# Kernel tuning notes

Measured on AMD Instinct MI355X. Metric: run time of the kernel, lower is better.

Reference implementation:

```python
import jax, jax.numpy as jnp
import numpy as np

NB, NLOC, NALL, NNEI = 1, 4096, 6144, 64
N_EDGE, N_ANGLE, A_SEL = 262144, 409600, 10
N_DIM, E_DIM, A_DIM, AXIS = 128, 64, 32, 4
SEL_REDUCE = 10.0


def _lin_params(key, din, dout):
    k1, k2 = jax.random.split(key)
    W = jax.random.normal(k1, (din, dout), jnp.float32) / np.float32(np.sqrt(din))
    b = jax.random.normal(k2, (dout,), jnp.float32) * 0.01
    return W, b


def setup_inputs():
    key = jax.random.key(0)
    ks = jax.random.split(key, 20)
    inp = {}
    inp["node_ebd_ext"] = jax.random.normal(ks[0], (NB, NALL, N_DIM), jnp.float32)
    inp["edge_ebd"] = jax.random.normal(ks[1], (N_EDGE, E_DIM), jnp.float32)
    inp["h2"] = jax.random.normal(ks[2], (N_EDGE, 3), jnp.float32)
    inp["angle_ebd"] = jax.random.normal(ks[3], (N_ANGLE, A_DIM), jnp.float32)
    inp["nlist"] = jax.random.randint(ks[4], (NB, NLOC, NNEI), 0, NALL)
    inp["nlist_mask"] = jnp.ones((NB, NLOC, NNEI), jnp.bool_)
    inp["sw"] = jax.random.uniform(ks[5], (N_EDGE,), jnp.float32)
    inp["a_nlist"] = jax.random.randint(ks[6], (NB, NLOC, A_SEL), 0, NALL)
    inp["a_nlist_mask"] = jnp.ones((NB, NLOC, A_SEL), jnp.bool_)
    inp["a_sw"] = jax.random.uniform(ks[7], (N_ANGLE,), jnp.float32)
    n2e = jax.random.randint(ks[8], (N_EDGE,), 0, NB * NLOC)
    n_ext2e = jax.random.randint(ks[9], (N_EDGE,), 0, NB * NALL)
    inp["edge_index"] = jnp.stack([n2e, n_ext2e])
    n2a = jax.random.randint(ks[10], (N_ANGLE,), 0, NB * NLOC)
    eij2a = jax.random.randint(ks[11], (N_ANGLE,), 0, N_EDGE)
    eik2a = jax.random.randint(ks[12], (N_ANGLE,), 0, N_EDGE)
    inp["angle_index"] = jnp.stack([n2a, eij2a, eik2a])
    sym_dim = (N_DIM + E_DIM) * AXIS          # 768
    edge_info_dim = 2 * N_DIM + E_DIM         # 320
    angle_dim = A_DIM + N_DIM + 2 * E_DIM     # 288
    inp["W_node_self"], inp["b_node_self"] = _lin_params(ks[13], N_DIM, N_DIM)
    inp["W_node_sym"], inp["b_node_sym"] = _lin_params(ks[14], sym_dim, N_DIM)
    inp["W_node_edge"], inp["b_node_edge"] = _lin_params(ks[15], edge_info_dim, N_DIM)
    inp["W_edge_self"], inp["b_edge_self"] = _lin_params(ks[16], edge_info_dim, E_DIM)
    inp["W_edge_angle1"], inp["b_edge_angle1"] = _lin_params(ks[17], angle_dim, E_DIM)
    inp["W_edge_angle2"], inp["b_edge_angle2"] = _lin_params(ks[18], E_DIM, E_DIM)
    inp["W_angle_self"], inp["b_angle_self"] = _lin_params(ks[19], angle_dim, A_DIM)
    inp["n_res0"] = jnp.full((N_DIM,), 0.1, jnp.float32)
    inp["n_res1"] = jnp.full((N_DIM,), 0.1, jnp.float32)
    inp["n_res2"] = jnp.full((N_DIM,), 0.1, jnp.float32)
    inp["e_res0"] = jnp.full((E_DIM,), 0.1, jnp.float32)
    inp["e_res1"] = jnp.full((E_DIM,), 0.1, jnp.float32)
    inp["a_res0"] = jnp.full((A_DIM,), 0.1, jnp.float32)
    return inp


def reference(node_ebd_ext, edge_ebd, h2, angle_ebd, nlist, nlist_mask, sw,
              a_nlist, a_nlist_mask, a_sw, edge_index, angle_index,
              W_node_self, b_node_self, W_node_sym, b_node_sym,
              W_node_edge, b_node_edge, W_edge_self, b_edge_self,
              W_edge_angle1, b_edge_angle1, W_edge_angle2, b_edge_angle2,
              W_angle_self, b_angle_self,
              n_res0, n_res1, n_res2, e_res0, e_res1, a_res0):
    act = jax.nn.silu
    nb, nloc, nnei = nlist.shape
    n_dim = node_ebd_ext.shape[-1]
    n_edge = h2.shape[0]
    dyn_e_sel = nnei / SEL_REDUCE
    dyn_a_sel = a_nlist.shape[-1] / SEL_REDUCE
    node_ebd = node_ebd_ext[:, :nloc]
    n2e, n_ext2e = edge_index[0], edge_index[1]
    n2a, eij2a, eik2a = angle_index[0], angle_index[1], angle_index[2]
    nei_node_ebd = node_ebd_ext.reshape(-1, n_dim)[n_ext2e]  # [n_edge, n_dim]
    node_self = act(node_ebd @ W_node_self + b_node_self)

    def sym_op(flat_ebd):
        # symmetrization: outer(h2, sw*ebd) scattered to owners, then grrg
        d = flat_ebd.shape[-1]
        w = flat_ebd * sw[:, None]
        h2g2 = jax.ops.segment_sum(
            (h2[:, :, None] * w[:, None, :]).reshape(n_edge, 3 * d),
            n2e, num_segments=nb * nloc)
        h2g2 = h2g2.reshape(nb, nloc, 3, d) * (dyn_e_sel ** -0.5)
        m = h2g2[..., :AXIS]  # [nb, nloc, 3, axis]
        g = jnp.einsum('blxa,blxd->blad', m, h2g2) / 3.0
        return g.reshape(nb, nloc, AXIS * d)

    sym_edge = sym_op(edge_ebd)
    sym_node = sym_op(nei_node_ebd)
    node_sym = act(jnp.concatenate([sym_edge, sym_node], -1) @ W_node_sym + b_node_sym)
    node_i = node_ebd.reshape(-1, n_dim)[n2e]
    edge_info = jnp.concatenate([node_i, nei_node_ebd, edge_ebd], -1)  # [n_edge, 320]
    node_edge_update = act(edge_info @ W_node_edge + b_node_edge) * sw[:, None]
    node_edge_msg = jax.ops.segment_sum(node_edge_update, n2e, num_segments=nb * nloc).reshape(nb, nloc, -1) / dyn_e_sel
    n_updated = node_ebd + n_res0 * node_self + n_res1 * node_sym + n_res2 * node_edge_msg
    edge_self = act(edge_info @ W_edge_self + b_edge_self)
    node_for_angle = node_ebd.reshape(-1, n_dim)[n2a]
    edge_ik = edge_ebd[eik2a]
    edge_ij = edge_ebd[eij2a]
    angle_info = jnp.concatenate([angle_ebd, node_for_angle, edge_ik, edge_ij], -1)  # [n_angle, 288]
    edge_angle = act(angle_info @ W_edge_angle1 + b_edge_angle1)
    reduced = jax.ops.segment_sum(edge_angle * a_sw[:, None], eij2a, num_segments=n_edge) / (dyn_a_sel ** 0.5)
    edge_angle_msg = act(reduced @ W_edge_angle2 + b_edge_angle2)
    e_updated = edge_ebd + e_res0 * edge_self + e_res1 * edge_angle_msg
    angle_self = act(angle_info @ W_angle_self + b_angle_self)
    a_updated = angle_ebd + a_res0 * angle_self
    return (n_updated, e_updated, a_updated)
```

## Files before the change

### kernel.cpp

```cpp
#include <hip/hip_runtime.h>
#include <hip/hip_bf16.h>

#define NLOC_   4096
#define NALL_   6144
#define NEDGE_  262144
#define NANGLE_ 409600

typedef __bf16 bf16x8 __attribute__((ext_vector_type(8)));
typedef float  f32x4  __attribute__((ext_vector_type(4)));
typedef unsigned short u16;

__device__ __forceinline__ float silu_(float x){ return x / (1.0f + __expf(-x)); }

__device__ __forceinline__ u16 f2bu(float f){
    union { float f; unsigned u; } v; v.f = f;
    unsigned r = v.u + 0x7fffu + ((v.u >> 16) & 1u);
    return (u16)(r >> 16);
}
__device__ __forceinline__ float bu2f(u16 b){
    union { unsigned u; float f; } v; v.u = ((unsigned)b) << 16; return v.f;
}
__device__ __forceinline__ void st_bf16x4(u16* dst, float4 v){
    unsigned lo = (unsigned)f2bu(v.x) | ((unsigned)f2bu(v.y) << 16);
    unsigned hi = (unsigned)f2bu(v.z) | ((unsigned)f2bu(v.w) << 16);
    *reinterpret_cast<uint2*>(dst) = make_uint2(lo, hi);
}

__global__ __launch_bounds__(256) void k_mega_prep(
    const float* __restrict__ Wne, const float* __restrict__ Wes,
    const float* __restrict__ W1,  const float* __restrict__ WA,
    const float* __restrict__ W2,  const float* __restrict__ Wsym,
    const float* __restrict__ Wns,
    const float* __restrict__ node_ext, const float* __restrict__ edge_ebd,
    const float* __restrict__ angle_ebd,
    const int* __restrict__ n2e, const int* __restrict__ eij2a,
    u16* __restrict__ WTe, u16* __restrict__ WTa2, u16* __restrict__ WTaN,
    u16* __restrict__ WT2, u16* __restrict__ WsymT, u16* __restrict__ WnsT,
    u16* __restrict__ NB, u16* __restrict__ EB, u16* __restrict__ AB,
    int* __restrict__ cnt, int* __restrict__ cnt2)
{
    const int b = blockIdx.x, tid = threadIdx.x;
    if (b < 812) {
        int i = b*256 + tid;
        if (i < 61440) {
            int r = i/320, c = i - r*320;
            WTe[i] = f2bu(r < 128 ? Wne[c*128 + r] : Wes[c*64 + (r-128)]);
        } else if (i < 76800) {
            int j = i - 61440; int r = j/160, c2 = j - r*160;
            int k = (c2 < 32) ? c2 : c2 + 128;
            WTa2[j] = f2bu(r < 64 ? W1[k*64 + r] : WA[k*32 + (r-64)]);
        } else if (i < 89088) {
            int j = i - 76800; int r = j >> 7, c2 = j & 127;
            int k = c2 + 32;
            WTaN[j] = f2bu(r < 64 ? W1[k*64 + r] : WA[k*32 + (r-64)]);
        } else if (i < 93184) {
            int j = i - 89088; int r = j >> 6, c = j & 63;
            WT2[j] = f2bu(W2[c*64 + r]);
        } else if (i < 191488) {
            int j = i - 93184; int r = j/768, c = j - r*768;
            WsymT[j] = f2bu(Wsym[c*128 + r]);
        } else {
            int j = i - 191488; int r = j >> 7, c = j & 127;
            WnsT[j] = f2bu(Wns[c*128 + r]);
        }
    } else if (b < 1580) {
        int i = (b - 812)*256 + tid;
        float4 v = ((const float4*)node_ext)[i];
        st_bf16x4(&NB[(size_t)i*4], v);
    } else if (b < 3628) {
        for (int i = (b - 1580)*256 + tid; i < NEDGE_*64/4; i += 2048*256) {
            float4 v = ((const float4*)edge_ebd)[i];
            st_bf16x4(&EB[(size_t)i*4], v);
        }
    } else if (b < 5676) {
        for (int i = (b - 3628)*256 + tid; i < NANGLE_*32/4; i += 2048*256) {
            float4 v = ((const float4*)angle_ebd)[i];
            st_bf16x4(&AB[(size_t)i*4], v);
        }
    } else if (b < 6700) {
        int e = (b - 5676)*256 + tid;
        atomicAdd(&cnt[n2e[e]], 1);
    } else {
        int a = (b - 6700)*256 + tid;
        atomicAdd(&cnt2[eij2a[a]], 1);
    }
}

__global__ __launch_bounds__(256) void k_scan_misc(
    const int* __restrict__ cnt, int* __restrict__ off, int* __restrict__ cursor,
    const int* __restrict__ cnt2, int* __restrict__ bsum,
    const u16* __restrict__ NB, const u16* __restrict__ WTe,
    const u16* __restrict__ WTaN,
    float* __restrict__ nconst, float* __restrict__ nconstA)
{
    __shared__ __align__(16) u16 sN[64][136];
    int* wa = (int*)&sN[0][0];
    const int b = blockIdx.x, t = threadIdx.x;

    if (b == 0) {
        int v[16]; int s = 0;
        #pragma unroll
        for (int k = 0; k < 16; ++k) { v[k] = s; s += cnt[16*t + k]; }
        wa[t] = s;
        __syncthreads();
        for (int d = 1; d < 256; d <<= 1) {
            int x = wa[t];
            int y = (t >= d) ? wa[t-d] : 0;
            __syncthreads();
            wa[t] = x + y;
            __syncthreads();
        }
        int excl = (t == 0) ? 0 : wa[t-1];
        #pragma unroll
        for (int k = 0; k < 16; ++k) {
            off[16*t + k]    = excl + v[k];
            cursor[16*t + k] = excl + v[k];
        }
        if (t == 255) off[4096] = excl + s;
    } else if (b <= 256) {
        int bb = b - 1;
        int4 v = ((const int4*)cnt2)[bb*256 + t];
        wa[t] = v.x + v.y + v.z + v.w;
        __syncthreads();
        for (int d = 128; d > 0; d >>= 1) {
            if (t < d) wa[t] += wa[t+d];
            __syncthreads();
        }
        if (t == 0) bsum[bb] = wa[0];
    } else if (b <= 320) {
        const int e0 = (b - 257) * 64;
        #pragma unroll
        for (int f = t; f < 1024; f += 256) {
            int r = f >> 4, c = f & 15;
            *(uint4*)&sN[r][8*c] = ((const uint4*)&NB[(size_t)(e0 + r)*128])[c];
        }
        __syncthreads();
// ... 52 lines not shown
            #pragma unroll
            for (int j = 0; j < 4; ++j) {
                int r = 16*w + 4*hq + j;
                nconstA[(size_t)(n0 + r)*96 + c] = acc[nf][j];
            }
        }
    }
}

__global__ void k_scan2b(const int* __restrict__ bsum, int* __restrict__ boff)
{
    __shared__ int wa[256];
    int t = threadIdx.x;
    wa[t] = bsum[t];
    __syncthreads();
    for (int d = 1; d < 256; d <<= 1) {
        int x = wa[t];
        int y = (t >= d) ? wa[t-d] : 0;
        __syncthreads();
        wa[t] = x + y;
        __syncthreads();
    }
    boff[t] = (t == 0) ? 0 : wa[t-1];
}

__global__ void k_scan2c(const int* __restrict__ cnt2, const int* __restrict__ boff,
                         int* __restrict__ off2, int* __restrict__ cursor2)
{
    __shared__ int wa[256];
    int b = blockIdx.x, t = threadIdx.x;
    int4 v = ((const int4*)cnt2)[b*256 + t];
    int s1 = v.x, s2 = s1 + v.y, s3 = s2 + v.z, s4 = s3 + v.w;
    wa[t] = s4;
    __syncthreads();
    for (int d = 1; d < 256; d <<= 1) {
        int x = wa[t];
        int y = (t >= d) ? wa[t-d] : 0;
        __syncthreads();
        wa[t] = x + y;
        __syncthreads();
    }
    int base = boff[b] + ((t == 0) ? 0 : wa[t-1]);
    int i = (b*256 + t)*4;
    off2[i]   = base;      cursor2[i]   = base;
    off2[i+1] = base + s1; cursor2[i+1] = base + s1;
    off2[i+2] = base + s2; cursor2[i+2] = base + s2;
    off2[i+3] = base + s3; cursor2[i+3] = base + s3;
    if (b == 255 && t == 255) off2[NEDGE_] = NANGLE_;
}

__global__ void k_fill2(const int* __restrict__ n2e, int* __restrict__ cursor,
                        int* __restrict__ csr,
                        const int* __restrict__ eij2a, int* __restrict__ cursor2,
                        int* __restrict__ csr2)
{
    int b = blockIdx.x;
    if (b < 1024) {
        int e = b*256 + threadIdx.x;
        int pos = atomicAdd(&cursor[n2e[e]], 1);
        csr[pos] = e;
    } else {
        int a = (b - 1024)*256 + threadIdx.x;
        int pos = atomicAdd(&cursor2[eij2a[a]], 1);
        csr2[pos] = a;
    }
}

__global__ __launch_bounds__(256, 4) void k_edge_flat(
    const u16* __restrict__ NB, const u16* __restrict__ EB,
    const float* __restrict__ h2, const float* __restrict__ sw,
    const int* __restrict__ n2e, const int* __restrict__ n_ext2e,
    const int* __restrict__ csr,
    const u16* __restrict__ WTe, const float* __restrict__ nconst,
    const float* __restrict__ bne, const float* __restrict__ bes,
    float* __restrict__ msg,
    float* __restrict__ h2g2_e, float* __restrict__ h2g2_n,
    u16* __restrict__ eselfO)
{
    __shared__ __align__(16) u16 sA[64][200];
    __shared__ float sH[4][576];
    __shared__ int   s_eid[64];
    __shared__ int   s_node[64];
    __shared__ int   s_g[64];
    __shared__ float s_sw[64];
    __shared__ float s_h2[64][3];
    __shared__ int   s_segstart[65];
    __shared__ int   s_nseg;

    const int tid = threadIdx.x;
    const int w  = tid >> 6, l = tid & 63;
    const int lr = l & 15, hq = l >> 4, lk = hq * 8;
    const int base = blockIdx.x * 64;

    if (tid < 64) {
        int e = csr[base + tid];
        s_eid[tid]  = e;
        s_node[tid] = n2e[e];
        s_g[tid]    = n_ext2e[e];
        s_sw[tid]   = sw[e];
        s_h2[tid][0] = h2[e*3];
        s_h2[tid][1] = h2[e*3+1];
        s_h2[tid][2] = h2[e*3+2];
    }
    __syncthreads();

    if (tid < 64) {
        bool flag = (tid == 0) || (s_node[tid] != s_node[tid-1]);
        unsigned long long mask = __ballot(flag);
        if (flag) {
            int sid = __popcll(mask & ((1ull << tid) - 1ull));
            s_segstart[sid] = tid;
        }
        if (tid == 0) {
            int ns = __popcll(mask);
            s_nseg = ns;
            s_segstart[ns] = 64;
        }
    }

    #pragma unroll
    for (int f = tid; f < 1024; f += 256) {
        int r = f >> 4, c = f & 15;
        *(uint4*)&sA[r][8*c] = ((const uint4*)&NB[(size_t)s_g[r]*128])[c];
    }
    #pragma unroll
    for (int f = tid; f < 512; f += 256) {
        int r = f >> 3, c = f & 7;
        *(uint4*)&sA[r][128 + 8*c] = ((const uint4*)&EB[(size_t)s_eid[r]*64])[c];
    }
    __syncthreads();

    float bias[3];
    int   cful[3];
    #pragma unroll
    for (int nf = 0; nf < 3; ++nf) {
        int c = 48*w + 16*nf + lr;
        cful[nf] = c;
        bias[nf] = (c < 128) ? bne[c] : bes[c-128];
    }

    f32x4 acc[4][3] = {};
    #pragma unroll
    for (int kk = 0; kk < 6; ++kk) {
        bf16x8 a[4], b[3];
        #pragma unroll
        for (int m = 0; m < 4; ++m)
            a[m] = *(const bf16x8*)&sA[16*m + lr][kk*32 + lk];
        #pragma unroll
        for (int nf = 0; nf < 3; ++nf)
            b[nf] = *(const bf16x8*)&WTe[(size_t)cful[nf]*320 + 128 + kk*32 + lk];
        #pragma unroll
        for (int m = 0; m < 4; ++m)
            #pragma unroll
            for (int nf = 0; nf < 3; ++nf)
                acc[m][nf] = __builtin_amdgcn_mfma_f32_16x16x32_bf16(a[m], b[nf], acc[m][nf], 0, 0, 0);
    }

    #pragma unroll
    for (int nf = 0; nf < 3; ++nf) {
        int c = cful[nf];
        if (c < 128) {
            #pragma unroll
            for (int m = 0; m < 4; ++m)
                #pragma unroll
                for (int j = 0; j < 4; ++j) {
                    int r = 16*m + 4*hq + j;
                    float ncv = nconst[(size_t)s_node[r]*192 + c];
                    acc[m][nf][j] = silu_(acc[m][nf][j] + ncv + bias[nf]) * s_sw[r];
                }
        } else {
            int c2 = c - 128;
            #pragma unroll
            for (int m = 0; m < 4; ++m)
                #pragma unroll
                for (int j = 0; j < 4; ++j) {
                    int r = 16*m + 4*hq + j;
                    float ncv = nconst[(size_t)s_node[r]*192 + c];
                    eselfO[(size_t)s_eid[r]*64 + c2] =
                        f2bu(silu_(acc[m][nf][j] + ncv + bias[nf]));
                }
        }
    }

    const int nseg = s_nseg;
    for (int s = 0; s < nseg; ++s) {
        int rs = s_segstart[s], re = s_segstart[s+1];
        int nd = s_node[rs];
        #pragma unroll
        for (int nf = 0; nf < 3; ++nf) {
            if (cful[nf] >= 128) continue;
            float v = 0.f;
            #pragma unroll
            for (int m = 0; m < 4; ++m)
                #pragma unroll
                for (int j = 0; j < 4; ++j) {
                    int r = 16*m + 4*hq + j;
                    v += (r >= rs && r < re) ? acc[m][nf][j] : 0.f;
                }
            v += __shfl_xor(v, 16);
            v += __shfl_xor(v, 32);
            if (hq == 0) atomicAdd(&msg[(size_t)nd*128 + cful[nf]], v);
        }
    }

    for (int s = 0; s < nseg; ++s) {
        int rs = s_segstart[s], re = s_segstart[s+1];
        int nd = s_node[rs];
        int lo = max(16*w, rs), hi = min(16*w + 16, re);
        float hacc[9] = {0.f,0.f,0.f,0.f,0.f,0.f,0.f,0.f,0.f};
        for (int r = lo; r < hi; ++r) {
            float swv = s_sw[r];
            float s0 = s_h2[r][0] * swv;
            float s1 = s_h2[r][1] * swv;
            float s2 = s_h2[r][2] * swv;
            float eb = bu2f(sA[r][128 + l]);
            float n0 = bu2f(sA[r][l]);
            float n1 = bu2f(sA[r][64 + l]);
            hacc[0] = fmaf(s0, eb, hacc[0]);
            hacc[1] = fmaf(s1, eb, hacc[1]);
            hacc[2] = fmaf(s2, eb, hacc[2]);
            hacc[3] = fmaf(s0, n0, hacc[3]);
            hacc[4] = fmaf(s0, n1, hacc[4]);
            hacc[5] = fmaf(s1, n0, hacc[5]);
            hacc[6] = fmaf(s1, n1, hacc[6]);
            hacc[7] = fmaf(s2, n0, hacc[7]);
            hacc[8] = fmaf(s2, n1, hacc[8]);
        }
        #pragma unroll
        for (int q = 0; q < 3; ++q) sH[w][q*64 + l] = hacc[q];
        #pragma unroll
        for (int q = 0; q < 6; ++q) sH[w][192 + q*64 + l] = hacc[3+q];
        __syncthreads();
        for (int i = tid; i < 576; i += 256) {
            float v = sH[0][i] + sH[1][i] + sH[2][i] + sH[3][i];
            if (i < 192) atomicAdd(&h2g2_e[(size_t)nd*192 + i], v);
            else         atomicAdd(&h2g2_n[(size_t)nd*384 + (i - 192)], v);
        }
        __syncthreads();
    }
}

__global__ __launch_bounds__(256) void k_angle_mfma(
    const u16* __restrict__ EB, const u16* __restrict__ AB,
    const float* __restrict__ a_sw,
    const int* __restrict__ n2a, const int* __restrict__ eij2a,
    const int* __restrict__ eik2a, const int* __restrict__ csr2,
    const u16* __restrict__ WTa2, const float* __restrict__ nconstA,
    const float* __restrict__ b1, const float* __restrict__ bA,
    const float* __restrict__ a_res0,
    u16* __restrict__ ea, float* __restrict__ a_out)
{
    __shared__ __align__(16) u16 sA[32][168];
    __shared__ __align__(16) u16 sEA[32][64];
    __shared__ int s_a[32], s_nd[32], s_ij[32], s_ik[32];
    __shared__ float s_asw[32];
    const int tid = threadIdx.x;
    const int p0 = blockIdx.x * 32;

    if (tid < 32) {
        int a = csr2[p0 + tid];
        s_a[tid]  = a;
        s_nd[tid] = n2a[a];
        s_ij[tid] = eij2a[a];
        s_ik[tid] = eik2a[a];
        s_asw[tid] = a_sw[a];
    }
    __syncthreads();

    if (tid < 128) {
        int r = tid >> 2, c = tid & 3;
        *(uint4*)&sA[r][8*c] = ((const uint4*)&AB[(size_t)s_a[r]*32])[c];
    }
    {
        int r = tid >> 3, c = tid & 7;
        *(uint4*)&sA[r][32 + 8*c] = ((const uint4*)&EB[(size_t)s_ik[r]*64])[c];
        *(uint4*)&sA[r][96 + 8*c] = ((const uint4*)&EB[(size_t)s_ij[r]*64])[c];
    }
    __syncthreads();

    const int w = tid >> 6, l = tid & 63;
    const int lr = l & 15, hq = l >> 4, lk = hq * 8;
    const int mrow  = (w & 1) * 16;
    const int nbase = (w >> 1) * 48;

    f32x4 acc[3] = {};
    #pragma unroll
    for (int kk = 0; kk < 5; ++kk) {
        bf16x8 a = *(const bf16x8*)&sA[mrow + lr][kk*32 + lk];
        #pragma unroll
        for (int nf = 0; nf < 3; ++nf) {
            bf16x8 b = *(const bf16x8*)&WTa2[(size_t)(nbase + 16*nf + lr)*160 + kk*32 + lk];
            acc[nf] = __builtin_amdgcn_mfma_f32_16x16x32_bf16(a, b, acc[nf], 0, 0, 0);
        }
    }

    #pragma unroll
    for (int nf = 0; nf < 3; ++nf) {
        int c = nbase + 16*nf + lr;
        if (c < 64) {
            float bb = b1[c];
            #pragma unroll
            for (int j = 0; j < 4; ++j) {
                int r = mrow + 4*hq + j;
                float nca = nconstA[(size_t)s_nd[r]*96 + c];
                sEA[r][c] = f2bu(silu_(acc[nf][j] + nca + bb) * s_asw[r]);
            }
        } else {
            int c2 = c - 64;
            float bb = bA[c2], rr = a_res0[c2];
            #pragma unroll
            for (int j = 0; j < 4; ++j) {
                int r = mrow + 4*hq + j;
                float nca = nconstA[(size_t)s_nd[r]*96 + c];
                a_out[(size_t)s_a[r]*32 + c2] =
                    bu2f(sA[r][c2]) + rr * silu_(acc[nf][j] + nca + bb);
            }
        }
    }
    __syncthreads();

    {
        int r = tid >> 3, c = tid & 7;
        *(uint4*)&ea[((size_t)(p0 + r))*64 + 8*c] = *(const uint4*)&sEA[r][8*c];
    }
}

__global__ __launch_bounds__(256) void k_fin(
    const u16* __restrict__ EB, const u16* __restrict__ eselfO,
    const u16* __restrict__ ea, const int* __restrict__ off2,
    const u16* __restrict__ WT2,
    const float* __restrict__ b2_, const float* __restrict__ er0,
    const float* __restrict__ er1,
    float* __restrict__ e_out,
    const float* __restrict__ h2g2_e, const float* __restrict__ h2g2_n,
    u16* __restrict__ symcB)
{
    __shared__ __align__(16) u16 sR[64][72];
    __shared__ __align__(16) u16 sE[64][72];
    __shared__ __align__(16) u16 sB[64][72];
    const int tid = threadIdx.x;
    const int blk = blockIdx.x;

    if (blk < 4096) {
        const int e0 = blk * 64;
        const int w = tid >> 6, l = tid & 63;

        #pragma unroll
        for (int f = tid; f < 512; f += 256) {
            int r = f >> 3, c = f & 7;
            *(uint4*)&sB[r][8*c] = ((const uint4*)&EB[(size_t)(e0 + r)*64])[c];
            *(uint4*)&sE[r][8*c] = ((const uint4*)&eselfO[(size_t)(e0 + r)*64])[c];
        }

        #pragma unroll
        for (int r16 = 0; r16 < 16; ++r16) {
            int r = w*16 + r16;
            int e = e0 + r;
            float s = 0.f;
            int jb = off2[e], je = off2[e+1];
            for (int j = jb; j < je; ++j)
                s += bu2f(ea[(size_t)j*64 + l]);
            sR[r][l] = f2bu(s);
        }
        __syncthreads();

        const int lr = l & 15, hq = l >> 4, lk = hq * 8;
        f32x4 acc[4] = {};
        #pragma unroll
        for (int kk = 0; kk < 2; ++kk) {
            bf16x8 b = *(const bf16x8*)&WT2[(size_t)(16*w + lr)*64 + kk*32 + lk];
            #pragma unroll
            for (int m = 0; m < 4; ++m) {
                bf16x8 a = *(const bf16x8*)&sR[16*m + lr][kk*32 + lk];
                acc[m] = __builtin_amdgcn_mfma_f32_16x16x32_bf16(a, b, acc[m], 0, 0, 0);
            }
        }
// ... 110 lines not shown
            for (int j = 0; j < 4; ++j) {
                int r = 16*m + 4*hq + j;
                size_t idx = (size_t)(n0 + r)*128 + c;
                float self_ = silu_(accS[m][nf][j] + bS);
                float sym_  = silu_(accY[m][nf][j] + bY);
                n_out[idx] = node_ext[idx] + r0*self_ + r1*sym_
                           + r2 * msg[idx] * (1.0f / 6.4f);
            }
    }
}

extern "C" void kernel_launch(void* const* d_in, const int* in_sizes, int n_in,
                              void* d_out, int out_size, void* d_ws, size_t ws_size,
                              hipStream_t stream)
{
    const float* node_ext  = (const float*)d_in[0];
    const float* edge_ebd  = (const float*)d_in[1];
    const float* h2        = (const float*)d_in[2];
    const float* angle_ebd = (const float*)d_in[3];
    const float* sw        = (const float*)d_in[6];
    const float* a_sw      = (const float*)d_in[9];
    const int*  edge_index  = (const int*)d_in[10];
    const int*  angle_index = (const int*)d_in[11];
    const int* n2e     = edge_index;
    const int* n_ext2e = edge_index + NEDGE_;
    const int* n2a     = angle_index;
    const int* eij2a   = angle_index + NANGLE_;
    const int* eik2a   = angle_index + 2*NANGLE_;

    const float* Wns  = (const float*)d_in[12];
    const float* bns  = (const float*)d_in[13];
    const float* Wsym = (const float*)d_in[14];
    const float* bsym = (const float*)d_in[15];
    const float* Wne  = (const float*)d_in[16];
    const float* bne  = (const float*)d_in[17];
    const float* Wes  = (const float*)d_in[18];
    const float* bes  = (const float*)d_in[19];
    const float* W1   = (const float*)d_in[20];
    const float* b1   = (const float*)d_in[21];
    const float* W2   = (const float*)d_in[22];
    const float* b2_  = (const float*)d_in[23];
    const float* WA   = (const float*)d_in[24];
    const float* bA   = (const float*)d_in[25];
    const float* nr0  = (const float*)d_in[26];
    const float* nr1  = (const float*)d_in[27];
    const float* nr2  = (const float*)d_in[28];
    const float* er0  = (const float*)d_in[29];
    const float* er1  = (const float*)d_in[30];
    const float* ar0  = (const float*)d_in[31];

    char* wsp = (char*)d_ws;
    u16*   ea      = (u16*)wsp;    wsp += (size_t)NANGLE_ * 64 * 2;
    u16*   EB      = (u16*)wsp;    wsp += (size_t)NEDGE_ * 64 * 2;
    u16*   NB      = (u16*)wsp;    wsp += (size_t)NALL_ * 128 * 2;
    u16*   AB      = (u16*)wsp;    wsp += (size_t)NANGLE_ * 32 * 2;
    u16*   eselfO  = (u16*)wsp;    wsp += (size_t)NEDGE_ * 64 * 2;
    u16*   symcB   = (u16*)wsp;    wsp += (size_t)NLOC_ * 768 * 2;
    int*   cnt     = (int*)wsp;    wsp += 4096 * 4;
    int*   cnt2    = (int*)wsp;    wsp += (size_t)NEDGE_ * 4;
    float* msg     = (float*)wsp;  wsp += (size_t)NLOC_ * 128 * 4;
    float* h2g2_e  = (float*)wsp;  wsp += (size_t)NLOC_ * 192 * 4;
    float* h2g2_n  = (float*)wsp;  wsp += (size_t)NLOC_ * 384 * 4;
    size_t zero_bytes = 4096*4 + (size_t)NEDGE_*4 + (size_t)NLOC_*128*4
                      + (size_t)NLOC_*192*4 + (size_t)NLOC_*384*4;
    int*   off     = (int*)wsp;    wsp += 4104 * 4;
    int*   cursor  = (int*)wsp;    wsp += 4096 * 4;
    int*   csr     = (int*)wsp;    wsp += (size_t)NEDGE_ * 4;
    int*   off2    = (int*)wsp;    wsp += ((size_t)NEDGE_ + 16) * 4;
    int*   cursor2 = (int*)wsp;    wsp += (size_t)NEDGE_ * 4;
    int*   bsum    = (int*)wsp;    wsp += 256 * 4;
    int*   boff    = (int*)wsp;    wsp += 256 * 4;
    int*   csr2    = (int*)wsp;    wsp += (size_t)NANGLE_ * 4;
    float* nconst  = (float*)wsp;  wsp += (size_t)NLOC_ * 192 * 4;
    float* nconstA = (float*)wsp;  wsp += (size_t)NLOC_ * 96 * 4;
    u16*   WTe     = (u16*)wsp;    wsp += 192 * 320 * 2;
    u16*   WTa2    = (u16*)wsp;    wsp += 96 * 160 * 2;
    u16*   WTaN    = (u16*)wsp;    wsp += 96 * 128 * 2;
    u16*   WT2     = (u16*)wsp;    wsp += 64 * 64 * 2;
    u16*   WsymT   = (u16*)wsp;    wsp += 128 * 768 * 2;
    u16*   WnsT    = (u16*)wsp;    wsp += 128 * 128 * 2;

    hipMemsetAsync(cnt, 0, zero_bytes, stream);

    float* n_out = (float*)d_out;
    float* e_out = n_out + (size_t)NLOC_ * 128;
    float* a_out = e_out + (size_t)NEDGE_ * 64;

    k_mega_prep <<<8300, 256, 0, stream>>>(Wne, Wes, W1, WA, W2, Wsym, Wns,
                                           node_ext, edge_ebd, angle_ebd,
                                           n2e, eij2a,
                                           WTe, WTa2, WTaN, WT2, WsymT, WnsT,
                                           NB, EB, AB, cnt, cnt2);
    k_scan_misc <<<385, 256, 0, stream>>>(cnt, off, cursor, cnt2, bsum,
                                          NB, WTe, WTaN, nconst, nconstA);
    k_scan2b <<<1, 256, 0, stream>>>(bsum, boff);
    k_scan2c <<<256, 256, 0, stream>>>(cnt2, boff, off2, cursor2);
    k_fill2  <<<2624, 256, 0, stream>>>(n2e, cursor, csr, eij2a, cursor2, csr2);

    k_edge_flat <<<NEDGE_/64, 256, 0, stream>>>(NB, EB, h2, sw, n2e, n_ext2e, csr,
                                                WTe, nconst, bne, bes,
                                                msg, h2g2_e, h2g2_n, eselfO);
    k_angle_mfma <<<NANGLE_/32, 256, 0, stream>>>(EB, AB, a_sw,
                                                  n2a, eij2a, eik2a, csr2,
                                                  WTa2, nconstA, b1, bA, ar0,
                                                  ea, a_out);
    k_fin <<<8192, 256, 0, stream>>>(EB, eselfO, ea, off2, WT2, b2_, er0, er1,
                                     e_out, h2g2_e, h2g2_n, symcB);
    k_node_mfma <<<NLOC_/32, 256, 0, stream>>>(symcB, NB, node_ext, msg,
                                               WsymT, WnsT, bns, bsym,
                                               nr0, nr1, nr2, n_out);
}
```

Baseline: 422.6 us.

## Drop angle bf16 prepass, scatter edge rows in CSR order, stage nconst in LDS

Removes the separate bf16 conversion pass for angle embeddings; the angle kernel now converts gathered fp32 rows inline. The CSR fill kernel also copies each edge's bf16 row into a CSR-ordered buffer, so the edge kernel reads contiguous rows instead of gathering. The edge kernel computes segment IDs with a shuffle (removing one barrier) and caches per-segment nconst rows in reused LDS for up to 12 segments, falling back to global loads beyond that. The trade-offs are an extra 32MB scatter-copy, an extra barrier before sH is reused, and wider fp32 gathers in the angle kernel.

```diff
diff --git a/kernel.cpp b/kernel.cpp
--- a/kernel.cpp
+++ b/kernel.cpp
@@ -32,11 +32,10 @@
     const float* __restrict__ W2,  const float* __restrict__ Wsym,
     const float* __restrict__ Wns,
     const float* __restrict__ node_ext, const float* __restrict__ edge_ebd,
-    const float* __restrict__ angle_ebd,
     const int* __restrict__ n2e, const int* __restrict__ eij2a,
     u16* __restrict__ WTe, u16* __restrict__ WTa2, u16* __restrict__ WTaN,
     u16* __restrict__ WT2, u16* __restrict__ WsymT, u16* __restrict__ WnsT,
-    u16* __restrict__ NB, u16* __restrict__ EB, u16* __restrict__ AB,
+    u16* __restrict__ NB, u16* __restrict__ EB,
     int* __restrict__ cnt, int* __restrict__ cnt2)
 {
     const int b = blockIdx.x, tid = threadIdx.x;
@@ -72,16 +71,11 @@
             float4 v = ((const float4*)edge_ebd)[i];
             st_bf16x4(&EB[(size_t)i*4], v);
         }
-    } else if (b < 5676) {
-        for (int i = (b - 3628)*256 + tid; i < NANGLE_*32/4; i += 2048*256) {
-            float4 v = ((const float4*)angle_ebd)[i];
-            st_bf16x4(&AB[(size_t)i*4], v);
-        }
-    } else if (b < 6700) {
-        int e = (b - 5676)*256 + tid;
+    } else if (b < 4652) {
+        int e = (b - 3628)*256 + tid;
         atomicAdd(&cnt[n2e[e]], 1);
     } else {
-        int a = (b - 6700)*256 + tid;
+        int a = (b - 4652)*256 + tid;
         atomicAdd(&cnt2[eij2a[a]], 1);
     }
 }
@@ -240,13 +234,18 @@
 __global__ void k_fill2(const int* __restrict__ n2e, int* __restrict__ cursor,
                         int* __restrict__ csr,
                         const int* __restrict__ eij2a, int* __restrict__ cursor2,
-                        int* __restrict__ csr2)
+                        int* __restrict__ csr2,
+                        const u16* __restrict__ EB, u16* __restrict__ EBs)
 {
     int b = blockIdx.x;
     if (b < 1024) {
         int e = b*256 + threadIdx.x;
         int pos = atomicAdd(&cursor[n2e[e]], 1);
         csr[pos] = e;
+        const uint4* src = (const uint4*)&EB[(size_t)e*64];
+        uint4* dst = (uint4*)&EBs[(size_t)pos*64];
+        #pragma unroll
+        for (int c = 0; c < 8; ++c) dst[c] = src[c];
     } else {
         int a = (b - 1024)*256 + threadIdx.x;
         int pos = atomicAdd(&cursor2[eij2a[a]], 1);
@@ -255,7 +254,7 @@
 }
 
 __global__ __launch_bounds__(256, 4) void k_edge_flat(
-    const u16* __restrict__ NB, const u16* __restrict__ EB,
+    const u16* __restrict__ NB, const u16* __restrict__ EBs,
     const float* __restrict__ h2, const float* __restrict__ sw,
     const int* __restrict__ n2e, const int* __restrict__ n_ext2e,
     const int* __restrict__ csr,
@@ -266,13 +265,14 @@
     u16* __restrict__ eselfO)
 {
     __shared__ __align__(16) u16 sA[64][200];
-    __shared__ float sH[4][576];
+    __shared__ __align__(16) float sH[4][576];
     __shared__ int   s_eid[64];
     __shared__ int   s_node[64];
     __shared__ int   s_g[64];
     __shared__ float s_sw[64];
     __shared__ float s_h2[64][3];
     __shared__ int   s_segstart[65];
+    __shared__ int   s_segid[64];
     __shared__ int   s_nseg;
 
     const int tid = threadIdx.x;
@@ -282,29 +282,29 @@
 
     if (tid < 64) {
         int e = csr[base + tid];
+        int nd = n2e[e];
         s_eid[tid]  = e;
-        s_node[tid] = n2e[e];
+        s_node[tid] = nd;
         s_g[tid]    = n_ext2e[e];
         s_sw[tid]   = sw[e];
         s_h2[tid][0] = h2[e*3];
         s_h2[tid][1] = h2[e*3+1];
         s_h2[tid][2] = h2[e*3+2];
-    }
-    __syncthreads();
-
-    if (tid < 64) {
-        bool flag = (tid == 0) || (s_node[tid] != s_node[tid-1]);
+        int ndp = __shfl_up(nd, 1);
+        bool flag = (tid == 0) || (nd != ndp);
         unsigned long long mask = __ballot(flag);
         if (flag) {
             int sid = __popcll(mask & ((1ull << tid) - 1ull));
             s_segstart[sid] = tid;
         }
+        s_segid[tid] = __popcll(mask & ((1ull << tid) | ((1ull << tid) - 1ull))) - 1;
         if (tid == 0) {
             int ns = __popcll(mask);
             s_nseg = ns;
             s_segstart[ns] = 64;
         }
     }
+    __syncthreads();
 
     #pragma unroll
     for (int f = tid; f < 1024; f += 256) {
@@ -314,7 +314,15 @@
     #pragma unroll
     for (int f = tid; f < 512; f += 256) {
         int r = f >> 3, c = f & 7;
-        *(uint4*)&sA[r][128 + 8*c] = ((const uint4*)&EB[(size_t)s_eid[r]*64])[c];
+        *(uint4*)&sA[r][128 + 8*c] = ((const uint4*)&EBs[(size_t)(base + r)*64])[c];
+    }
+    {
+        float* sNC = (float*)&sH[0][0];
+        int nsg = min(s_nseg, 12);
+        for (int i = tid; i < nsg*192; i += 256) {
+            int sgi = i / 192, c = i - sgi*192;
+            sNC[i] = nconst[(size_t)s_node[s_segstart[sgi]]*192 + c];
+        }
     }
     __syncthreads();
 
@@ -344,6 +352,7 @@
                 acc[m][nf] = __builtin_amdgcn_mfma_f32_16x16x32_bf16(a[m], b[nf], acc[m][nf], 0, 0, 0);
     }
 
+    const float* sNC = (const float*)&sH[0][0];
     #pragma unroll
     for (int nf = 0; nf < 3; ++nf) {
         int c = cful[nf];
@@ -353,7 +362,10 @@
                 #pragma unroll
                 for (int j = 0; j < 4; ++j) {
                     int r = 16*m + 4*hq + j;
-                    float ncv = nconst[(size_t)s_node[r]*192 + c];
+                    int sgi = s_segid[r];
+                    float ncv;
+                    if (sgi < 12) ncv = sNC[sgi*192 + c];
+                    else          ncv = nconst[(size_t)s_node[r]*192 + c];
                     acc[m][nf][j] = silu_(acc[m][nf][j] + ncv + bias[nf]) * s_sw[r];
                 }
         } else {
@@ -363,7 +375,10 @@
                 #pragma unroll
                 for (int j = 0; j < 4; ++j) {
                     int r = 16*m + 4*hq + j;
-                    float ncv = nconst[(size_t)s_node[r]*192 + c];
+                    int sgi = s_segid[r];
+                    float ncv;
+                    if (sgi < 12) ncv = sNC[sgi*192 + c];
+                    else          ncv = nconst[(size_t)s_node[r]*192 + c];
                     eselfO[(size_t)s_eid[r]*64 + c2] =
                         f2bu(silu_(acc[m][nf][j] + ncv + bias[nf]));
                 }
@@ -390,6 +405,8 @@
             if (hq == 0) atomicAdd(&msg[(size_t)nd*128 + cful[nf]], v);
         }
     }
+
+    __syncthreads();
 
     for (int s = 0; s < nseg; ++s) {
         int rs = s_segstart[s], re = s_segstart[s+1];
@@ -429,7 +446,7 @@
 }
 
 __global__ __launch_bounds__(256) void k_angle_mfma(
-    const u16* __restrict__ EB, const u16* __restrict__ AB,
+    const u16* __restrict__ EB, const float* __restrict__ angle_ebd,
     const float* __restrict__ a_sw,
     const int* __restrict__ n2a, const int* __restrict__ eij2a,
     const int* __restrict__ eik2a, const int* __restrict__ csr2,
@@ -455,9 +472,9 @@
     }
     __syncthreads();
 
-    if (tid < 128) {
-        int r = tid >> 2, c = tid & 3;
-        *(uint4*)&sA[r][8*c] = ((const uint4*)&AB[(size_t)s_a[r]*32])[c];
+    {
+        int r = tid >> 3, c = tid & 7;
+        st_bf16x4(&sA[r][4*c], ((const float4*)angle_ebd)[(size_t)s_a[r]*8 + c]);
     }
     {
         int r = tid >> 3, c = tid & 7;
@@ -726,8 +743,8 @@
     char* wsp = (char*)d_ws;
     u16*   ea      = (u16*)wsp;    wsp += (size_t)NANGLE_ * 64 * 2;
     u16*   EB      = (u16*)wsp;    wsp += (size_t)NEDGE_ * 64 * 2;
+    u16*   EBs     = (u16*)wsp;    wsp += (size_t)NEDGE_ * 64 * 2;
     u16*   NB      = (u16*)wsp;    wsp += (size_t)NALL_ * 128 * 2;
-    u16*   AB      = (u16*)wsp;    wsp += (size_t)NANGLE_ * 32 * 2;
     u16*   eselfO  = (u16*)wsp;    wsp += (size_t)NEDGE_ * 64 * 2;
     u16*   symcB   = (u16*)wsp;    wsp += (size_t)NLOC_ * 768 * 2;
     int*   cnt     = (int*)wsp;    wsp += 4096 * 4;
@@ -760,21 +777,22 @@
     float* e_out = n_out + (size_t)NLOC_ * 128;
     float* a_out = e_out + (size_t)NEDGE_ * 64;
 
-    k_mega_prep <<<8300, 256, 0, stream>>>(Wne, Wes, W1, WA, W2, Wsym, Wns,
-                                           node_ext, edge_ebd, angle_ebd,
+    k_mega_prep <<<6252, 256, 0, stream>>>(Wne, Wes, W1, WA, W2, Wsym, Wns,
+                                           node_ext, edge_ebd,
                                            n2e, eij2a,
                                            WTe, WTa2, WTaN, WT2, WsymT, WnsT,
-                                           NB, EB, AB, cnt, cnt2);
+                                           NB, EB, cnt, cnt2);
     k_scan_misc <<<385, 256, 0, stream>>>(cnt, off, cursor, cnt2, bsum,
                                           NB, WTe, WTaN, nconst, nconstA);
     k_scan2b <<<1, 256, 0, stream>>>(bsum, boff);
     k_scan2c <<<256, 256, 0, stream>>>(cnt2, boff, off2, cursor2);
-    k_fill2  <<<2624, 256, 0, stream>>>(n2e, cursor, csr, eij2a, cursor2, csr2);
-
-    k_edge_flat <<<NEDGE_/64, 256, 0, stream>>>(NB, EB, h2, sw, n2e, n_ext2e, csr,
+    k_fill2  <<<2624, 256, 0, stream>>>(n2e, cursor, csr, eij2a, cursor2, csr2,
+                                        EB, EBs);
+
+    k_edge_flat <<<NEDGE_/64, 256, 0, stream>>>(NB, EBs, h2, sw, n2e, n_ext2e, csr,
                                                 WTe, nconst, bne, bes,
                                                 msg, h2g2_e, h2g2_n, eselfO);
-    k_angle_mfma <<<NANGLE_/32, 256, 0, stream>>>(EB, AB, a_sw,
+    k_angle_mfma <<<NANGLE_/32, 256, 0, stream>>>(EB, angle_ebd, a_sw,
                                                   n2a, eij2a, eik2a, csr2,
                                                   WTa2, nconstA, b1, bA, ar0,
                                                   ea, a_out);
```

After: 459.9 us. +8.8%, slower.

## Merge edge and angle kernels into one interleaved launch, drop angle bf16 precast

Applied to the files above, without the earlier changes.

Fuses the edge-message kernel and the angle MFMA kernel into a single launch whose blocks are interleaved (one edge block per three angle blocks, then trailing angle blocks). Angle embeddings are now read as fp32 directly and converted to bf16 while being staged into shared memory, so the separate bf16 copy of angle_ebd in the prep kernel and its workspace buffer are removed. This saves one kernel launch and a full read and write of the angle tensor, and lets the two workloads overlap on the GPU. In exchange, the angle blocks now carry the edge kernel's larger shared-memory footprint and register budget, which may lower their occupancy.

```diff
diff --git a/kernel.cpp b/kernel.cpp
--- a/kernel.cpp
+++ b/kernel.cpp
@@ -32,11 +32,10 @@
     const float* __restrict__ W2,  const float* __restrict__ Wsym,
     const float* __restrict__ Wns,
     const float* __restrict__ node_ext, const float* __restrict__ edge_ebd,
-    const float* __restrict__ angle_ebd,
     const int* __restrict__ n2e, const int* __restrict__ eij2a,
     u16* __restrict__ WTe, u16* __restrict__ WTa2, u16* __restrict__ WTaN,
     u16* __restrict__ WT2, u16* __restrict__ WsymT, u16* __restrict__ WnsT,
-    u16* __restrict__ NB, u16* __restrict__ EB, u16* __restrict__ AB,
+    u16* __restrict__ NB, u16* __restrict__ EB,
     int* __restrict__ cnt, int* __restrict__ cnt2)
 {
     const int b = blockIdx.x, tid = threadIdx.x;
@@ -72,16 +71,11 @@
             float4 v = ((const float4*)edge_ebd)[i];
             st_bf16x4(&EB[(size_t)i*4], v);
         }
-    } else if (b < 5676) {
-        for (int i = (b - 3628)*256 + tid; i < NANGLE_*32/4; i += 2048*256) {
-            float4 v = ((const float4*)angle_ebd)[i];
-            st_bf16x4(&AB[(size_t)i*4], v);
-        }
-    } else if (b < 6700) {
-        int e = (b - 5676)*256 + tid;
+    } else if (b < 4652) {
+        int e = (b - 3628)*256 + tid;
         atomicAdd(&cnt[n2e[e]], 1);
     } else {
-        int a = (b - 6700)*256 + tid;
+        int a = (b - 4652)*256 + tid;
         atomicAdd(&cnt2[eij2a[a]], 1);
     }
 }
@@ -254,7 +248,7 @@
     }
 }
 
-__global__ __launch_bounds__(256, 4) void k_edge_flat(
+__global__ __launch_bounds__(256, 4) void k_edge_angle(
     const u16* __restrict__ NB, const u16* __restrict__ EB,
     const float* __restrict__ h2, const float* __restrict__ sw,
     const int* __restrict__ n2e, const int* __restrict__ n_ext2e,
@@ -263,10 +257,17 @@
     const float* __restrict__ bne, const float* __restrict__ bes,
     float* __restrict__ msg,
     float* __restrict__ h2g2_e, float* __restrict__ h2g2_n,
-    u16* __restrict__ eselfO)
+    u16* __restrict__ eselfO,
+    const float* __restrict__ angle_ebd, const float* __restrict__ a_sw,
+    const int* __restrict__ n2a, const int* __restrict__ eij2a,
+    const int* __restrict__ eik2a, const int* __restrict__ csr2,
+    const u16* __restrict__ WTa2, const float* __restrict__ nconstA,
+    const float* __restrict__ b1, const float* __restrict__ bA,
+    const float* __restrict__ a_res0,
+    u16* __restrict__ ea, float* __restrict__ a_out)
 {
     __shared__ __align__(16) u16 sA[64][200];
-    __shared__ float sH[4][576];
+    __shared__ __align__(16) float sH[4][576];
     __shared__ int   s_eid[64];
     __shared__ int   s_node[64];
     __shared__ int   s_g[64];
@@ -274,242 +275,238 @@
     __shared__ float s_h2[64][3];
     __shared__ int   s_segstart[65];
     __shared__ int   s_nseg;
+    __shared__ int   s_a[32], s_nd[32], s_ij[32], s_ik[32];
+    __shared__ float s_asw[32];
 
     const int tid = threadIdx.x;
+    const int b = blockIdx.x;
+    bool isEdge; int widx;
+    if (b < 16384) {
+        if ((b & 3) == 0) { isEdge = true;  widx = b >> 2; }
+        else              { isEdge = false; widx = b - (b >> 2) - 1; }
+    } else { isEdge = false; widx = 12288 + (b - 16384); }
+
     const int w  = tid >> 6, l = tid & 63;
     const int lr = l & 15, hq = l >> 4, lk = hq * 8;
-    const int base = blockIdx.x * 64;
-
-    if (tid < 64) {
-        int e = csr[base + tid];
-        s_eid[tid]  = e;
-        s_node[tid] = n2e[e];
-        s_g[tid]    = n_ext2e[e];
-        s_sw[tid]   = sw[e];
-        s_h2[tid][0] = h2[e*3];
-        s_h2[tid][1] = h2[e*3+1];
-        s_h2[tid][2] = h2[e*3+2];
-    }
-    __syncthreads();
-
-    if (tid < 64) {
-        bool flag = (tid == 0) || (s_node[tid] != s_node[tid-1]);
-        unsigned long long mask = __ballot(flag);
-        if (flag) {
-            int sid = __popcll(mask & ((1ull << tid) - 1ull));
-            s_segstart[sid] = tid;
-        }
-        if (tid == 0) {
-            int ns = __popcll(mask);
-            s_nseg = ns;
-            s_segstart[ns] = 64;
-        }
-    }
-
-    #pragma unroll
-    for (int f = tid; f < 1024; f += 256) {
-        int r = f >> 4, c = f & 15;
-        *(uint4*)&sA[r][8*c] = ((const uint4*)&NB[(size_t)s_g[r]*128])[c];
-    }
-    #pragma unroll
-    for (int f = tid; f < 512; f += 256) {
-        int r = f >> 3, c = f & 7;
-        *(uint4*)&sA[r][128 + 8*c] = ((const uint4*)&EB[(size_t)s_eid[r]*64])[c];
-    }
-    __syncthreads();
-
-    float bias[3];
-    int   cful[3];
-    #pragma unroll
-    for (int nf = 0; nf < 3; ++nf) {
-        int c = 48*w + 16*nf + lr;
-        cful[nf] = c;
-        bias[nf] = (c < 128) ? bne[c] : bes[c-128];
-    }
-
-    f32x4 acc[4][3] = {};
-    #pragma unroll
-    for (int kk = 0; kk < 6; ++kk) {
-        bf16x8 a[4], b[3];
-        #pragma unroll
-        for (int m = 0; m < 4; ++m)
-            a[m] = *(const bf16x8*)&sA[16*m + lr][kk*32 + lk];
-        #pragma unroll
-        for (int nf = 0; nf < 3; ++nf)
-            b[nf] = *(const bf16x8*)&WTe[(size_t)cful[nf]*320 + 128 + kk*32 + lk];
-        #pragma unroll
-        for (int m = 0; m < 4; ++m)
+
+    if (isEdge) {
+        const int base = widx * 64;
+
+        if (tid < 64) {
+            int e = csr[base + tid];
+            s_eid[tid]  = e;
+            s_node[tid] = n2e[e];
+            s_g[tid]    = n_ext2e[e];
+            s_sw[tid]   = sw[e];
+            s_h2[tid][0] = h2[e*3];
+            s_h2[tid][1] = h2[e*3+1];
+            s_h2[tid][2] = h2[e*3+2];
+        }
+        __syncthreads();
+
+        if (tid < 64) {
+            bool flag = (tid == 0) || (s_node[tid] != s_node[tid-1]);
+            unsigned long long mask = __ballot(flag);
+            if (flag) {
+                int sid = __popcll(mask & ((1ull << tid) - 1ull));
+                s_segstart[sid] = tid;
+            }
+            if (tid == 0) {
+                int ns = __popcll(mask);
+                s_nseg = ns;
+                s_segstart[ns] = 64;
+            }
+        }
+
+        #pragma unroll
+        for (int f = tid; f < 1024; f += 256) {
+            int r = f >> 4, c = f & 15;
+            *(uint4*)&sA[r][8*c] = ((const uint4*)&NB[(size_t)s_g[r]*128])[c];
+        }
+        #pragma unroll
+        for (int f = tid; f < 512; f += 256) {
+            int r = f >> 3, c = f & 7;
+            *(uint4*)&sA[r][128 + 8*c] = ((const uint4*)&EB[(size_t)s_eid[r]*64])[c];
+        }
+        __syncthreads();
+
+        float bias[3];
+        int   cful[3];
+        #pragma unroll
+        for (int nf = 0; nf < 3; ++nf) {
+            int c = 48*w + 16*nf + lr;
+            cful[nf] = c;
+            bias[nf] = (c < 128) ? bne[c] : bes[c-128];
+        }
+
+        f32x4 acc[4][3] = {};
+        #pragma unroll
+        for (int kk = 0; kk < 6; ++kk) {
+            bf16x8 a[4], bb[3];
+            #pragma unroll
+            for (int m = 0; m < 4; ++m)
+                a[m] = *(const bf16x8*)&sA[16*m + lr][kk*32 + lk];
             #pragma unroll
             for (int nf = 0; nf < 3; ++nf)
-                acc[m][nf] = __builtin_amdgcn_mfma_f32_16x16x32_bf16(a[m], b[nf], acc[m][nf], 0, 0, 0);
-    }
-
-    #pragma unroll
-    for (int nf = 0; nf < 3; ++nf) {
-        int c = cful[nf];
-        if (c < 128) {
+                bb[nf] = *(const bf16x8*)&WTe[(size_t)cful[nf]*320 + 128 + kk*32 + lk];
             #pragma unroll
             for (int m = 0; m < 4; ++m)
                 #pragma unroll
+                for (int nf = 0; nf < 3; ++nf)
+                    acc[m][nf] = __builtin_amdgcn_mfma_f32_16x16x32_bf16(a[m], bb[nf], acc[m][nf], 0, 0, 0);
+        }
+
+        #pragma unroll
+        for (int nf = 0; nf < 3; ++nf) {
+            int c = cful[nf];
+            if (c < 128) {
+                #pragma unroll
+                for (int m = 0; m < 4; ++m)
+                    #pragma unroll
+                    for (int j = 0; j < 4; ++j) {
+                        int r = 16*m + 4*hq + j;
+                        float ncv = nconst[(size_t)s_node[r]*192 + c];
+                        acc[m][nf][j] = silu_(acc[m][nf][j] + ncv + bias[nf]) * s_sw[r];
+                    }
+            } else {
+                int c2 = c - 128;
+                #pragma unroll
+                for (int m = 0; m < 4; ++m)
+                    #pragma unroll
+                    for (int j = 0; j < 4; ++j) {
+                        int r = 16*m + 4*hq + j;
+                        float ncv = nconst[(size_t)s_node[r]*192 + c];
+                        eselfO[(size_t)s_eid[r]*64 + c2] =
+                            f2bu(silu_(acc[m][nf][j] + ncv + bias[nf]));
+                    }
+            }
+        }
+
+        const int nseg = s_nseg;
+        for (int s = 0; s < nseg; ++s) {
+            int rs = s_segstart[s], re = s_segstart[s+1];
+            int nd = s_node[rs];
+            #pragma unroll
+            for (int nf = 0; nf < 3; ++nf) {
+                if (cful[nf] >= 128) continue;
+                float v = 0.f;
+                #pragma unroll
+                for (int m = 0; m < 4; ++m)
+                    #pragma unroll
+                    for (int j = 0; j < 4; ++j) {
+                        int r = 16*m + 4*hq + j;
+                        v += (r >= rs && r < re) ? acc[m][nf][j] : 0.f;
+                    }
+                v += __shfl_xor(v, 16);
+                v += __shfl_xor(v, 32);
+                if (hq == 0) atomicAdd(&msg[(size_t)nd*128 + cful[nf]], v);
+            }
+        }
+
+        for (int s = 0; s < nseg; ++s) {
+            int rs = s_segstart[s], re = s_segstart[s+1];
+            int nd = s_node[rs];
+            int lo = max(16*w, rs), hi = min(16*w + 16, re);
+            float hacc[9] = {0.f,0.f,0.f,0.f,0.f,0.f,0.f,0.f,0.f};
+            for (int r = lo; r < hi; ++r) {
+                float swv = s_sw[r];
+                float s0 = s_h2[r][0] * swv;
+                float s1 = s_h2[r][1] * swv;
+                float s2 = s_h2[r][2] * swv;
+                float eb = bu2f(sA[r][128 + l]);
+                float n0 = bu2f(sA[r][l]);
+                float n1 = bu2f(sA[r][64 + l]);
+                hacc[0] = fmaf(s0, eb, hacc[0]);
+                hacc[1] = fmaf(s1, eb, hacc[1]);
+                hacc[2] = fmaf(s2, eb, hacc[2]);
+                hacc[3] = fmaf(s0, n0, hacc[3]);
+                hacc[4] = fmaf(s0, n1, hacc[4]);
+                hacc[5] = fmaf(s1, n0, hacc[5]);
+                hacc[6] = fmaf(s1, n1, hacc[6]);
+                hacc[7] = fmaf(s2, n0, hacc[7]);
+                hacc[8] = fmaf(s2, n1, hacc[8]);
+            }
+            #pragma unroll
+            for (int q = 0; q < 3; ++q) sH[w][q*64 + l] = hacc[q];
+            #pragma unroll
+            for (int q = 0; q < 6; ++q) sH[w][192 + q*64 + l] = hacc[3+q];
+            __syncthreads();
+            for (int i = tid; i < 576; i += 256) {
+                float v = sH[0][i] + sH[1][i] + sH[2][i] + sH[3][i];
+                if (i < 192) atomicAdd(&h2g2_e[(size_t)nd*192 + i], v);
+                else         atomicAdd(&h2g2_n[(size_t)nd*384 + (i - 192)], v);
+            }
+            __syncthreads();
+        }
+    } else {
+        u16 (*sA32)[168] = (u16(*)[168])&sA[0][0];
+        u16 (*sEA)[64]   = (u16(*)[64])&sH[0][0];
+        const int p0 = widx * 32;
+
+        if (tid < 32) {
+            int a = csr2[p0 + tid];
+            s_a[tid]  = a;
+            s_nd[tid] = n2a[a];
+            s_ij[tid] = eij2a[a];
+            s_ik[tid] = eik2a[a];
+            s_asw[tid] = a_sw[a];
+        }
+        __syncthreads();
+
+        {
+            int r = tid >> 3, c = tid & 7;
+            st_bf16x4(&sA32[r][4*c], ((const float4*)angle_ebd)[(size_t)s_a[r]*8 + c]);
+        }
+        {
+            int r = tid >> 3, c = tid & 7;
+            *(uint4*)&sA32[r][32 + 8*c] = ((const uint4*)&EB[(size_t)s_ik[r]*64])[c];
+            *(uint4*)&sA32[r][96 + 8*c] = ((const uint4*)&EB[(size_t)s_ij[r]*64])[c];
+        }
+        __syncthreads();
+
+        const int mrow  = (w & 1) * 16;
+        const int nbase = (w >> 1) * 48;
+
+        f32x4 acc[3] = {};
+        #pragma unroll
+        for (int kk = 0; kk < 5; ++kk) {
+            bf16x8 a = *(const bf16x8*)&sA32[mrow + lr][kk*32 + lk];
+            #pragma unroll
+            for (int nf = 0; nf < 3; ++nf) {
+                bf16x8 bb = *(const bf16x8*)&WTa2[(size_t)(nbase + 16*nf + lr)*160 + kk*32 + lk];
+                acc[nf] = __builtin_amdgcn_mfma_f32_16x16x32_bf16(a, bb, acc[nf], 0, 0, 0);
+            }
+        }
+
+        #pragma unroll
+        for (int nf = 0; nf < 3; ++nf) {
+            int c = nbase + 16*nf + lr;
+            if (c < 64) {
+                float bb = b1[c];
+                #pragma unroll
                 for (int j = 0; j < 4; ++j) {
-                    int r = 16*m + 4*hq + j;
-                    float ncv = nconst[(size_t)s_node[r]*192 + c];
-                    acc[m][nf][j] = silu_(acc[m][nf][j] + ncv + bias[nf]) * s_sw[r];
+                    int r = mrow + 4*hq + j;
+                    float nca = nconstA[(size_t)s_nd[r]*96 + c];
+                    sEA[r][c] = f2bu(silu_(acc[nf][j] + nca + bb) * s_asw[r]);
                 }
-        } else {
-            int c2 = c - 128;
-            #pragma unroll
-            for (int m = 0; m < 4; ++m)
+            } else {
+                int c2 = c - 64;
+                float bb = bA[c2], rr = a_res0[c2];
                 #pragma unroll
                 for (int j = 0; j < 4; ++j) {
-                    int r = 16*m + 4*hq + j;
-                    float ncv = nconst[(size_t)s_node[r]*192 + c];
-                    eselfO[(size_t)s_eid[r]*64 + c2] =
-                        f2bu(silu_(acc[m][nf][j] + ncv + bias[nf]));
+                    int r = mrow + 4*hq + j;
+                    float nca = nconstA[(size_t)s_nd[r]*96 + c];
+                    a_out[(size_t)s_a[r]*32 + c2] =
+                        bu2f(sA32[r][c2]) + rr * silu_(acc[nf][j] + nca + bb);
                 }
-        }
-    }
-
-    const int nseg = s_nseg;
-    for (int s = 0; s < nseg; ++s) {
-        int rs = s_segstart[s], re = s_segstart[s+1];
-        int nd = s_node[rs];
-        #pragma unroll
-        for (int nf = 0; nf < 3; ++nf) {
-            if (cful[nf] >= 128) continue;
-            float v = 0.f;
-            #pragma unroll
-            for (int m = 0; m < 4; ++m)
-                #pragma unroll
-                for (int j = 0; j < 4; ++j) {
-                    int r = 16*m + 4*hq + j;
-                    v += (r >= rs && r < re) ? acc[m][nf][j] : 0.f;
-                }
-            v += __shfl_xor(v, 16);
-            v += __shfl_xor(v, 32);
-            if (hq == 0) atomicAdd(&msg[(size_t)nd*128 + cful[nf]], v);
-        }
-    }
-
-    for (int s = 0; s < nseg; ++s) {
-        int rs = s_segstart[s], re = s_segstart[s+1];
-        int nd = s_node[rs];
-        int lo = max(16*w, rs), hi = min(16*w + 16, re);
-        float hacc[9] = {0.f,0.f,0.f,0.f,0.f,0.f,0.f,0.f,0.f};
-        for (int r = lo; r < hi; ++r) {
-            float swv = s_sw[r];
-            float s0 = s_h2[r][0] * swv;
-            float s1 = s_h2[r][1] * swv;
-            float s2 = s_h2[r][2] * swv;
-            float eb = bu2f(sA[r][128 + l]);
-            float n0 = bu2f(sA[r][l]);
-            float n1 = bu2f(sA[r][64 + l]);
-            hacc[0] = fmaf(s0, eb, hacc[0]);
-            hacc[1] = fmaf(s1, eb, hacc[1]);
-            hacc[2] = fmaf(s2, eb, hacc[2]);
-            hacc[3] = fmaf(s0, n0, hacc[3]);
-            hacc[4] = fmaf(s0, n1, hacc[4]);
-            hacc[5] = fmaf(s1, n0, hacc[5]);
-            hacc[6] = fmaf(s1, n1, hacc[6]);
-            hacc[7] = fmaf(s2, n0, hacc[7]);
-            hacc[8] = fmaf(s2, n1, hacc[8]);
-        }
-        #pragma unroll
-        for (int q = 0; q < 3; ++q) sH[w][q*64 + l] = hacc[q];
-        #pragma unroll
-        for (int q = 0; q < 6; ++q) sH[w][192 + q*64 + l] = hacc[3+q];
-        __syncthreads();
-        for (int i = tid; i < 576; i += 256) {
-            float v = sH[0][i] + sH[1][i] + sH[2][i] + sH[3][i];
-            if (i < 192) atomicAdd(&h2g2_e[(size_t)nd*192 + i], v);
-            else         atomicAdd(&h2g2_n[(size_t)nd*384 + (i - 192)], v);
-        }
-        __syncthreads();
-    }
-}
-
-__global__ __launch_bounds__(256) void k_angle_mfma(
-    const u16* __restrict__ EB, const u16* __restrict__ AB,
-    const float* __restrict__ a_sw,
-    const int* __restrict__ n2a, const int* __restrict__ eij2a,
-    const int* __restrict__ eik2a, const int* __restrict__ csr2,
-    const u16* __restrict__ WTa2, const float* __restrict__ nconstA,
-    const float* __restrict__ b1, const float* __restrict__ bA,
-    const float* __restrict__ a_res0,
-    u16* __restrict__ ea, float* __restrict__ a_out)
-{
-    __shared__ __align__(16) u16 sA[32][168];
-    __shared__ __align__(16) u16 sEA[32][64];
-    __shared__ int s_a[32], s_nd[32], s_ij[32], s_ik[32];
-    __shared__ float s_asw[32];
-    const int tid = threadIdx.x;
-    const int p0 = blockIdx.x * 32;
-
-    if (tid < 32) {
-        int a = csr2[p0 + tid];
-        s_a[tid]  = a;
-        s_nd[tid] = n2a[a];
-        s_ij[tid] = eij2a[a];
-        s_ik[tid] = eik2a[a];
-        s_asw[tid] = a_sw[a];
-    }
-    __syncthreads();
-
-    if (tid < 128) {
-        int r = tid >> 2, c = tid & 3;
-        *(uint4*)&sA[r][8*c] = ((const uint4*)&AB[(size_t)s_a[r]*32])[c];
-    }
-    {
-        int r = tid >> 3, c = tid & 7;
-        *(uint4*)&sA[r][32 + 8*c] = ((const uint4*)&EB[(size_t)s_ik[r]*64])[c];
-        *(uint4*)&sA[r][96 + 8*c] = ((const uint4*)&EB[(size_t)s_ij[r]*64])[c];
-    }
-    __syncthreads();
-
-    const int w = tid >> 6, l = tid & 63;
-    const int lr = l & 15, hq = l >> 4, lk = hq * 8;
-    const int mrow  = (w & 1) * 16;
-    const int nbase = (w >> 1) * 48;
-
-    f32x4 acc[3] = {};
-    #pragma unroll
-    for (int kk = 0; kk < 5; ++kk) {
-        bf16x8 a = *(const bf16x8*)&sA[mrow + lr][kk*32 + lk];
-        #pragma unroll
-        for (int nf = 0; nf < 3; ++nf) {
-            bf16x8 b = *(const bf16x8*)&WTa2[(size_t)(nbase + 16*nf + lr)*160 + kk*32 + lk];
-            acc[nf] = __builtin_amdgcn_mfma_f32_16x16x32_bf16(a, b, acc[nf], 0, 0, 0);
-        }
-    }
-
-    #pragma unroll
-    for (int nf = 0; nf < 3; ++nf) {
-        int c = nbase + 16*nf + lr;
-        if (c < 64) {
-            float bb = b1[c];
-            #pragma unroll
-            for (int j = 0; j < 4; ++j) {
-                int r = mrow + 4*hq + j;
-                float nca = nconstA[(size_t)s_nd[r]*96 + c];
-                sEA[r][c] = f2bu(silu_(acc[nf][j] + nca + bb) * s_asw[r]);
-            }
-        } else {
-            int c2 = c - 64;
-            float bb = bA[c2], rr = a_res0[c2];
-            #pragma unroll
-            for (int j = 0; j < 4; ++j) {
-                int r = mrow + 4*hq + j;
-                float nca = nconstA[(size_t)s_nd[r]*96 + c];
-                a_out[(size_t)s_a[r]*32 + c2] =
-                    bu2f(sA[r][c2]) + rr * silu_(acc[nf][j] + nca + bb);
-            }
-        }
-    }
-    __syncthreads();
-
-    {
-        int r = tid >> 3, c = tid & 7;
-        *(uint4*)&ea[((size_t)(p0 + r))*64 + 8*c] = *(const uint4*)&sEA[r][8*c];
+            }
+        }
+        __syncthreads();
+
+        {
+            int r = tid >> 3, c = tid & 7;
+            *(uint4*)&ea[((size_t)(p0 + r))*64 + 8*c] = *(const uint4*)&sEA[r][8*c];
+        }
     }
 }
 
@@ -727,7 +724,6 @@
     u16*   ea      = (u16*)wsp;    wsp += (size_t)NANGLE_ * 64 * 2;
     u16*   EB      = (u16*)wsp;    wsp += (size_t)NEDGE_ * 64 * 2;
     u16*   NB      = (u16*)wsp;    wsp += (size_t)NALL_ * 128 * 2;
-    u16*   AB      = (u16*)wsp;    wsp += (size_t)NANGLE_ * 32 * 2;
     u16*   eselfO  = (u16*)wsp;    wsp += (size_t)NEDGE_ * 64 * 2;
     u16*   symcB   = (u16*)wsp;    wsp += (size_t)NLOC_ * 768 * 2;
     int*   cnt     = (int*)wsp;    wsp += 4096 * 4;
@@ -760,24 +756,24 @@
     float* e_out = n_out + (size_t)NLOC_ * 128;
     float* a_out = e_out + (size_t)NEDGE_ * 64;
 
-    k_mega_prep <<<8300, 256, 0, stream>>>(Wne, Wes, W1, WA, W2, Wsym, Wns,
-                                           node_ext, edge_ebd, angle_ebd,
+    k_mega_prep <<<6252, 256, 0, stream>>>(Wne, Wes, W1, WA, W2, Wsym, Wns,
+                                           node_ext, edge_ebd,
                                            n2e, eij2a,
                                            WTe, WTa2, WTaN, WT2, WsymT, WnsT,
-                                           NB, EB, AB, cnt, cnt2);
+                                           NB, EB, cnt, cnt2);
     k_scan_misc <<<385, 256, 0, stream>>>(cnt, off, cursor, cnt2, bsum,
                                           NB, WTe, WTaN, nconst, nconstA);
     k_scan2b <<<1, 256, 0, stream>>>(bsum, boff);
     k_scan2c <<<256, 256, 0, stream>>>(cnt2, boff, off2, cursor2);
     k_fill2  <<<2624, 256, 0, stream>>>(n2e, cursor, csr, eij2a, cursor2, csr2);
 
-    k_edge_flat <<<NEDGE_/64, 256, 0, stream>>>(NB, EB, h2, sw, n2e, n_ext2e, csr,
-                                                WTe, nconst, bne, bes,
-                                                msg, h2g2_e, h2g2_n, eselfO);
-    k_angle_mfma <<<NANGLE_/32, 256, 0, stream>>>(EB, AB, a_sw,
-                                                  n2a, eij2a, eik2a, csr2,
-                                                  WTa2, nconstA, b1, bA, ar0,
-                                                  ea, a_out);
+    k_edge_angle <<<16896, 256, 0, stream>>>(NB, EB, h2, sw, n2e, n_ext2e, csr,
+                                             WTe, nconst, bne, bes,
+                                             msg, h2g2_e, h2g2_n, eselfO,
+                                             angle_ebd, a_sw,
+                                             n2a, eij2a, eik2a, csr2,
+                                             WTa2, nconstA, b1, bA, ar0,
+                                             ea, a_out);
     k_fin <<<8192, 256, 0, stream>>>(EB, eselfO, ea, off2, WT2, b2_, er0, er1,
                                      e_out, h2g2_e, h2g2_n, symcB);
     k_node_mfma <<<NLOC_/32, 256, 0, stream>>>(symcB, NB, node_ext, msg,
```

Measured after the change: 529.2 us. 25.2% more time.
